# Kernel tuning notes

Measured on AMD Instinct MI355X. Metric: run time of the kernel, lower is better.

The kernel has to match this reference:

```python
import jax, jax.numpy as jnp
import numpy as np

B, N, K, D, L = 8, 1024, 16, 256, 3  # batch, max_node_num, neighbor fan-in, g_hidden_dim, layers


def setup_inputs() -> dict:
    key = jax.random.key(0)
    ks = jax.random.split(key, 14)
    f32 = jnp.float32
    scale = 1.0 / np.sqrt(D).astype(np.float32)
    randn = lambda k, s: jax.random.normal(k, s, dtype=f32)
    lens = jax.random.randint(ks[12], (B,), N // 2, N + 1)
    node_mask = (jnp.arange(N)[None, :] < lens[:, None]).astype(f32)
    return {
        "h0": randn(ks[0], (B, N, D)),
        "c0": randn(ks[1], (B, N, D)),
        "x_in": randn(ks[2], (B, N, D)),
        "x_out": randn(ks[3], (B, N, D)),
        "W_in": randn(ks[4], (4, D, D)) * scale,   # gates stacked: [i, o, f, cell]
        "U_in": randn(ks[5], (4, D, D)) * scale,
        "W_out": randn(ks[6], (4, D, D)) * scale,
        "U_out": randn(ks[7], (4, D, D)) * scale,
        "b": jnp.zeros((4, D), dtype=f32),
        "in_mask": jax.random.randint(ks[8], (B, N, K), 0, 2).astype(f32),
        "out_mask": jax.random.randint(ks[9], (B, N, K), 0, 2).astype(f32),
        "node_mask": node_mask,
        "in_nodes": jax.random.randint(ks[10], (B, N, K), 0, N, dtype=jnp.int32),
        "out_nodes": jax.random.randint(ks[11], (B, N, K), 0, N, dtype=jnp.int32),
        "num_layers": L,
    }


def _gather_agg(h, idx, nb_mask, node_mask):
    # h: [B,N,D], idx: [B,N,K] -> masked sum of neighbor hidden states [B,N,D]
    nb = jax.vmap(lambda hb, ib: hb[ib])(h, idx)           # [B,N,K,D]
    agg = jnp.einsum('bnkd,bnk->bnd', nb, nb_mask)
    return agg * node_mask[..., None]


def reference(h0, c0, x_in, x_out, W_in, U_in, W_out, U_out, b,
              in_mask, out_mask, node_mask, in_nodes, out_nodes, num_layers):
    h, c = h0, c0
    nm = node_mask[..., None]
    for _ in range(num_layers):
        h_in = _gather_agg(h, in_nodes, in_mask, node_mask)
        h_out = _gather_agg(h, out_nodes, out_mask, node_mask)
        # pre-activation for all 4 gates at once: [4,B,N,D]
        pre = (jnp.einsum('bnd,gde->gbne', x_in, W_in)
               + jnp.einsum('bnd,gde->gbne', h_in, U_in)
               + jnp.einsum('bnd,gde->gbne', x_out, W_out)
               + jnp.einsum('bnd,gde->gbne', h_out, U_out)
               + b[:, None, None, :])
        i_g = jax.nn.sigmoid(pre[0])
        o_g = jax.nn.sigmoid(pre[1])
        f_g = jax.nn.sigmoid(pre[2])
        g = jnp.tanh(pre[3])
        c = (f_g * c + i_g * g) * nm
        h = o_g * jnp.tanh(c) * nm
    return h
```

## Files before the change

### kernel.cpp

```cpp
#include <hip/hip_runtime.h>
#include <hip/hip_bf16.h>
#include <cstdint>
#include <cstddef>

typedef __hip_bfloat16 bf16;
typedef _Float16 f16;
typedef __attribute__((ext_vector_type(4))) float f32x4;
typedef __attribute__((ext_vector_type(8))) _Float16 f16x8;
typedef __attribute__((ext_vector_type(4))) _Float16 f16x4;
typedef __attribute__((ext_vector_type(4))) unsigned short u16x4;

#define BB 8
#define NN 1024
#define KK 16
#define DD 256
#define MM (BB * NN)
#define NLAYER 3

__device__ __forceinline__ float ldf(const void* p, size_t i, int isf32) {
  return isf32 ? ((const float*)p)[i] : __bfloat162float(((const bf16*)p)[i]);
}

__device__ __forceinline__ f32x4 ldf4(const void* p, size_t vi, int isf32) {
  f32x4 r;
  if (isf32) {
    r = ((const f32x4*)p)[vi];
  } else {
    u16x4 u = ((const u16x4*)p)[vi];
#pragma unroll
    for (int q = 0; q < 4; q++) {
      union { unsigned u; float f; } c;
      c.u = ((unsigned)u[q]) << 16;
      r[q] = c.f;
    }
  }
  return r;
}

__device__ __forceinline__ void gload_lds16(const void* g, void* l) {
  __builtin_amdgcn_global_load_lds(
      (const __attribute__((address_space(1))) unsigned int*)g,
      (__attribute__((address_space(3))) unsigned int*)l, 16, 0, 0);
}

__device__ __forceinline__ int detect_isf32_wave(const void* W) {
  int lane = threadIdx.x & 63;
  unsigned short b = ((const unsigned short*)W)[2 * lane];
  int e = (b >> 7) & 0xFF;
  int sane = ((e >= 105 && e <= 130) || (b & 0x7FFF) == 0) ? 1 : 0;
  unsigned long long m = __ballot(sane);
  return (__popcll(m) > 32) ? 0 : 1;
}

__device__ __forceinline__ float fsigmoid(float x) {
  float a = fminf(fmaxf(-1.44269504f * x, -126.f), 126.f);
  float e = __builtin_amdgcn_exp2f(a);
  return __builtin_amdgcn_rcpf(1.f + e);
}
__device__ __forceinline__ float ftanh(float x) {
  float a = fminf(fmaxf(2.88539008f * x, -126.f), 126.f);
  float e = __builtin_amdgcn_exp2f(a);
  return 1.f - 2.f * __builtin_amdgcn_rcpf(1.f + e);
}

struct Params {
  const void *h0, *c0, *x_in, *x_out, *W_in, *U_in, *W_out, *U_out, *bvec;
  const void *in_mask, *out_mask, *node_mask;
  const int *in_nodes, *out_nodes;
  float *biasI, *nmF, *inmF, *outmF;
  f16 *h_cur, *c_cur, *A_buf, *X_buf, *BT_W, *BT_U, *XW;
  void* outp;
};

#define PREP_VEC_TOTAL (256 + 2048 + 32768 + 32768 + 524288 + 524288)
#define PREP_BLOCKS (256 + (PREP_VEC_TOTAL + 255) / 256)
__global__ void prep_k(Params p) {
  __shared__ float tile[64][65];
  int isf32 = detect_isf32_wave(p.W_in);
  int b = blockIdx.x;
  int t = threadIdx.x;

  if (b < 256) {
    int bx = b & 3, by = (b >> 2) & 3, z = b >> 4;
    int g = z & 3, which = z >> 2;
    const void* src = (which == 0) ? p.W_in : (which == 1) ? p.W_out
                     : (which == 2) ? p.U_in : p.U_out;
    f16* dst = (which < 2) ? p.BT_W : p.BT_U;
    int colofs = (which & 1) * 256;
    size_t gbase = (size_t)g * DD * DD;
    int tx = t & 63, ty = t >> 6;
    int d0 = bx * 64, e0 = by * 64;
#pragma unroll
    for (int r = 0; r < 64; r += 4)
      tile[ty + r][tx] = ldf(src, gbase + (size_t)(d0 + ty + r) * DD + e0 + tx, isf32);
    __syncthreads();
#pragma unroll
    for (int r = 0; r < 64; r += 4)
      dst[(size_t)(4 * (e0 + ty + r) + g) * 512 + colofs + d0 + tx] = (f16)tile[tx][ty + r];
    return;
  }

  size_t i = (size_t)(b - 256) * 256 + t;
  const size_t V0 = 256;
  const size_t V1 = V0 + 2048;
  const size_t V2 = V1 + 32768;
  const size_t V3 = V2 + 32768;
  const size_t V4 = V3 + 524288;
  const size_t V5 = V4 + 524288;
  if (i < V0) {
    f32x4 r;
#pragma unroll
    for (int g = 0; g < 4; g++) r[g] = ldf(p.bvec, (size_t)g * 256 + i, isf32);
    ((f32x4*)p.biasI)[i] = r;
  } else if (i < V1) {
    ((f32x4*)p.nmF)[i - V0] = ldf4(p.node_mask, i - V0, isf32);
  } else if (i < V2) {
    ((f32x4*)p.inmF)[i - V1] = ldf4(p.in_mask, i - V1, isf32);
  } else if (i < V3) {
    ((f32x4*)p.outmF)[i - V2] = ldf4(p.out_mask, i - V2, isf32);
  } else if (i < V4) {
    size_t j = i - V3;
    f32x4 hv = ldf4(p.h0, j, isf32);
    f32x4 cv = ldf4(p.c0, j, isf32);
    f16x4 ho, co;
#pragma unroll
    for (int q = 0; q < 4; q++) { ho[q] = (f16)hv[q]; co[q] = (f16)cv[q]; }
    ((f16x4*)p.h_cur)[j] = ho;
    ((f16x4*)p.c_cur)[j] = co;
  } else if (i < V5) {
    size_t j = i - V4;
    size_t m = j >> 6, d4 = (j & 63) * 4;
    f32x4 xi = ldf4(p.x_in, j, isf32);
    f32x4 xo = ldf4(p.x_out, j, isf32);
    f16x4 a, bq;
#pragma unroll
    for (int q = 0; q < 4; q++) { a[q] = (f16)xi[q]; bq[q] = (f16)xo[q]; }
    *(f16x4*)(p.X_buf + m * 512 + d4)       = a;
    *(f16x4*)(p.X_buf + m * 512 + 256 + d4) = bq;
  }
}

__global__ void gather_k(Params p) {
  int wave = threadIdx.x >> 6;
  int lane = threadIdx.x & 63;
  int m = (blockIdx.x & 7) * 1024 + (blockIdx.x >> 3) * 4 + wave;
  int l5 = lane & 31, dir = lane >> 5;
  int myidx = 0; float mymask = 0.f;
  if (lane < 16)      { myidx = p.in_nodes[(size_t)m * KK + lane];
                        mymask = p.inmF[(size_t)m * KK + lane]; }
  else if (lane < 32) { myidx = p.out_nodes[(size_t)m * KK + lane - 16];
                        mymask = p.outmF[(size_t)m * KK + lane - 16]; }
  const f16* hb = p.h_cur + (size_t)(m >> 10) * NN * DD;
  float acc[8] = {};
#pragma unroll
  for (int k = 0; k < KK; k++) {
    int src = dir * 16 + k;
    int idxk = __shfl(myidx, src);
    float wk = __shfl(mymask, src);
    f16x8 v = *(const f16x8*)(hb + (size_t)idxk * DD + l5 * 8);
#pragma unroll
    for (int q = 0; q < 8; q++) acc[q] += wk * (float)v[q];
  }
  float nm = p.nmF[m];
  f16x8 o;
#pragma unroll
  for (int q = 0; q < 8; q++) o[q] = (f16)(acc[q] * nm);
  *(f16x8*)(p.A_buf + (size_t)m * 512 + dir * 256 + l5 * 8) = o;
}

__device__ __forceinline__ int mtile_of(int bx) { return (bx & 7) * 8 + (bx >> 3); }

template <int FIRST>
__global__ __launch_bounds__(256, 2)
void gemm_k(Params p, int last) {
  __shared__ __attribute__((aligned(16))) char smem[65536];
  float* tileF = (float*)smem;
  int isf32 = detect_isf32_wave(p.W_in);
  int t = threadIdx.x;
  int w = t >> 6, lane = t & 63;
  int wr = w >> 1, wc = w & 1;
  int row16 = lane & 15, kgrp = lane >> 4;
  int mBase = mtile_of(blockIdx.x) * 128, nBase = blockIdx.y * 128;

  int aoff[2][4], boff[2][4];
#pragma unroll
  for (int sub = 0; sub < 2; sub++) {
    int ch = ((sub * 4 + kgrp) ^ (row16 & 7)) * 8;
#pragma unroll
    for (int i = 0; i < 4; i++) aoff[sub][i] = (wr * 64 + 16 * i + row16) * 64 + ch;
#pragma unroll
    for (int j = 0; j < 4; j++) boff[sub][j] = (wc * 64 + 16 * j + row16) * 64 + ch;
  }
  int srow = t >> 3;
  int scol = ((t & 7) ^ (srow & 7)) * 8;
  const f16* gaH0 = p.A_buf + (size_t)(mBase + srow) * 512 + scol;
  const f16* gbU0 = p.BT_U + (size_t)(nBase + srow) * 512 + scol;
  const f16* gaX0 = p.X_buf + (size_t)(mBase + srow) * 512 + scol;
  const f16* gbW0 = p.BT_W + (size_t)(nBase + srow) * 512 + scol;

  const size_t xwkey = ((size_t)(blockIdx.y * 64 + blockIdx.x) * 256 + t) * 16;

  f32x4 acc[4][4];
  if (FIRST) {
#pragma unroll
    for (int i = 0; i < 4; i++)
#pragma unroll
      for (int j = 0; j < 4; j++) acc[i][j] = (f32x4){0.f, 0.f, 0.f, 0.f};
  } else {
    const f16x4* xw = (const f16x4*)p.XW + xwkey;
#pragma unroll
    for (int i = 0; i < 4; i++)
#pragma unroll
      for (int j = 0; j < 4; j++) {
        f16x4 v = xw[i * 4 + j];
#pragma unroll
        for (int r = 0; r < 4; r++) acc[i][j][r] = (float)v[r];
      }
  }

  const int NSTEP = FIRST ? 16 : 8;
  auto stage = [&](int it, int buf) {
    const f16* ga; const f16* gb; int kt;
    if (FIRST && it < 8) { ga = gaX0; gb = gbW0; kt = it * 64; }
    else                 { ga = gaH0; gb = gbU0; kt = (FIRST ? it - 8 : it) * 64; }
    f16* As = (f16*)(smem + buf * 32768);
    f16* Bs = (f16*)(smem + buf * 32768 + 16384);
#pragma unroll
    for (int q = 0; q < 4; q++)
      gload_lds16(ga + kt + (size_t)(32 * q) * 512, As + q * 2048 + t * 8);
#pragma unroll
    for (int q = 0; q < 4; q++)
      gload_lds16(gb + kt + (size_t)(32 * q) * 512, Bs + q * 2048 + t * 8);
  };

  stage(0, 0);
  __syncthreads();

#pragma unroll
  for (int it = 0; it < NSTEP; ++it) {
    int cur = it & 1;
    if (it < NSTEP - 1) stage(it + 1, cur ^ 1);
    f16* As = (f16*)(smem + cur * 32768);
    f16* Bs = (f16*)(smem + cur * 32768 + 16384);
#pragma unroll
    for (int sub = 0; sub < 2; sub++) {
      f16x8 af[4], bfr[4];
#pragma unroll
      for (int i = 0; i < 4; i++) af[i] = *(const f16x8*)(As + aoff[sub][i]);
#pragma unroll
      for (int j = 0; j < 4; j++) bfr[j] = *(const f16x8*)(Bs + boff[sub][j]);
#pragma unroll
      for (int i = 0; i < 4; i++)
#pragma unroll
        for (int j = 0; j < 4; j++)
          acc[i][j] = __builtin_amdgcn_mfma_f32_16x16x32_f16(af[i], bfr[j], acc[i][j], 0, 0, 0);
    }
    if (FIRST && it == 7) {
      float bb4[4];
#pragma unroll
      for (int j = 0; j < 4; j++) bb4[j] = p.biasI[nBase + wc * 64 + 16 * j + row16];
      f16x4* dst = (f16x4*)p.XW + xwkey;
#pragma unroll
      for (int i = 0; i < 4; i++)
#pragma unroll
        for (int j = 0; j < 4; j++) {
          f16x4 v;
#pragma unroll
          for (int r = 0; r < 4; r++) {
            acc[i][j][r] += bb4[j];
            v[r] = (f16)acc[i][j][r];
          }
          dst[i * 4 + j] = v;
        }
    }
    __syncthreads();
  }

#pragma unroll
  for (int pp = 0; pp < 2; pp++) {
    __syncthreads();
    if (wc == pp) {
#pragma unroll
      for (int i = 0; i < 4; i++)
#pragma unroll
        for (int j = 0; j < 4; j++) {
          int cl = 16 * j + row16;
#pragma unroll
          for (int r = 0; r < 4; r++) {
            int rr = wr * 64 + 16 * i + 4 * kgrp + r;
            int ch = (cl >> 2) ^ (rr & 7);
            tileF[rr * 64 + ch * 4 + (cl & 3)] = acc[i][j][r];
          }
        }
    }
    __syncthreads();
    int el = t & 15;
    int nb2 = nBase + 64 * pp;
    int eb = nb2 >> 2;
#pragma unroll
    for (int rep = 0; rep < 8; rep++) {
      int ml = rep * 16 + (t >> 4);
      int gm = mBase + ml;
      f32x4 vals = *(const f32x4*)(tileF + ml * 64 + ((el ^ (ml & 7))) * 4);
      float nm = p.nmF[gm];
      size_t ci = (size_t)gm * DD + eb + el;
      float cold = (float)p.c_cur[ci];
      float ig = fsigmoid(vals[0]);
      float og = fsigmoid(vals[1]);
      float fg = fsigmoid(vals[2]);
      float gg = ftanh(vals[3]);
      float cn = (fg * cold + ig * gg) * nm;
      float hn = og * ftanh(cn) * nm;
      p.c_cur[ci] = (f16)cn;
      p.h_cur[ci] = (f16)hn;
      if (last) {
        if (isf32) ((float*)p.outp)[ci] = hn;
        else       ((bf16*)p.outp)[ci] = __float2bfloat16(hn);
      }
    }
  }
}

extern "C" void kernel_launch(void* const* d_in, const int* in_sizes, int n_in,
                              void* d_out, int out_size, void* d_ws, size_t ws_size,
                              hipStream_t stream) {
  char* ws = (char*)d_ws;
  f16*   h_cur = (f16*)(ws + 256);
  f16*   c_cur = h_cur + (size_t)MM * DD;
  f16*   A_buf = c_cur + (size_t)MM * DD;
  f16*   X_buf = A_buf + (size_t)MM * 512;
  f16*   BT_W  = X_buf + (size_t)MM * 512;
  f16*   BT_U  = BT_W + (size_t)1024 * 512;
  f16*   XW    = BT_U + (size_t)1024 * 512;
  float* biasI = (float*)(XW + (size_t)MM * 1024);
  float* nmF   = biasI + 1024;
  float* inmF  = nmF + MM;
  float* outmF = inmF + (size_t)MM * KK;

  Params p;
  p.h0 = d_in[0]; p.c0 = d_in[1]; p.x_in = d_in[2]; p.x_out = d_in[3];
  p.W_in = d_in[4]; p.U_in = d_in[5]; p.W_out = d_in[6]; p.U_out = d_in[7];
  p.bvec = d_in[8]; p.in_mask = d_in[9]; p.out_mask = d_in[10]; p.node_mask = d_in[11];
  p.in_nodes = (const int*)d_in[12]; p.out_nodes = (const int*)d_in[13];
  p.biasI = biasI; p.nmF = nmF; p.inmF = inmF; p.outmF = outmF;
  p.h_cur = h_cur; p.c_cur = c_cur; p.A_buf = A_buf; p.X_buf = X_buf;
  p.BT_W = BT_W; p.BT_U = BT_U; p.XW = XW;
  p.outp = d_out;

  prep_k<<<PREP_BLOCKS, 256, 0, stream>>>(p);
  for (int l = 0; l < NLAYER; l++) {
    gather_k<<<MM / 4, 256, 0, stream>>>(p);
    if (l == 0) gemm_k<1><<<dim3(MM / 128, 8), 256, 0, stream>>>(p, l == NLAYER - 1);
    else        gemm_k<0><<<dim3(MM / 128, 8), 256, 0, stream>>>(p, l == NLAYER - 1);
  }
}
```

Before: 199.4 us.

## Fuse first-layer gather into prep and read masks and c0 directly from inputs

Folds the first layer's neighbor gather into the prep kernel, reading h0 directly in its original dtype, which removes one launch and the h0/c0 conversion pass. The float copies of the node, in and out masks are dropped; gather and the GEMM epilogue now read the masks through the dtype-aware loader. The first GEMM also reads c0 directly. This cuts prep-side memory traffic and one kernel launch, in exchange for wider uncoalesced fp32 gathers of h0 on the first layer.

```diff
diff --git a/kernel.cpp b/kernel.cpp
--- a/kernel.cpp
+++ b/kernel.cpp
@@ -9,6 +9,7 @@
 typedef __attribute__((ext_vector_type(8))) _Float16 f16x8;
 typedef __attribute__((ext_vector_type(4))) _Float16 f16x4;
 typedef __attribute__((ext_vector_type(4))) unsigned short u16x4;
+typedef __attribute__((ext_vector_type(8))) unsigned short u16x8;
 
 #define BB 8
 #define NN 1024
@@ -67,20 +68,77 @@
   const void *h0, *c0, *x_in, *x_out, *W_in, *U_in, *W_out, *U_out, *bvec;
   const void *in_mask, *out_mask, *node_mask;
   const int *in_nodes, *out_nodes;
-  float *biasI, *nmF, *inmF, *outmF;
+  float *biasI;
   f16 *h_cur, *c_cur, *A_buf, *X_buf, *BT_W, *BT_U, *XW;
   void* outp;
 };
 
-#define PREP_VEC_TOTAL (256 + 2048 + 32768 + 32768 + 524288 + 524288)
-#define PREP_BLOCKS (256 + (PREP_VEC_TOTAL + 255) / 256)
+template <int FIRST>
+__device__ __forceinline__ void gather_body(const Params& p, int b, int t, int isf32) {
+  int wave = t >> 6;
+  int lane = t & 63;
+  int m = (b & 7) * 1024 + (b >> 3) * 4 + wave;
+  int l5 = lane & 31, dir = lane >> 5;
+  int myidx = 0; float mymask = 0.f;
+  if (lane < 16)      { myidx = p.in_nodes[(size_t)m * KK + lane];
+                        mymask = ldf(p.in_mask, (size_t)m * KK + lane, isf32); }
+  else if (lane < 32) { myidx = p.out_nodes[(size_t)m * KK + lane - 16];
+                        mymask = ldf(p.out_mask, (size_t)m * KK + lane - 16, isf32); }
+  int bb = m >> 10;
+  float acc8[8] = {};
+#pragma unroll
+  for (int k = 0; k < KK; k++) {
+    int src = dir * 16 + k;
+    int idxk = __shfl(myidx, src);
+    float wk = __shfl(mymask, src);
+    if (FIRST) {
+      if (isf32) {
+        const float* hr = (const float*)p.h0 + ((size_t)bb * NN + idxk) * DD + l5 * 8;
+        f32x4 a = *(const f32x4*)hr, b2 = *(const f32x4*)(hr + 4);
+#pragma unroll
+        for (int q = 0; q < 4; q++) { acc8[q] += wk * a[q]; acc8[4 + q] += wk * b2[q]; }
+      } else {
+        const unsigned short* hr =
+            (const unsigned short*)p.h0 + ((size_t)bb * NN + idxk) * DD + l5 * 8;
+        u16x8 v = *(const u16x8*)hr;
+#pragma unroll
+        for (int q = 0; q < 8; q++) {
+          union { unsigned u; float f; } c; c.u = ((unsigned)v[q]) << 16;
+          acc8[q] += wk * c.f;
+        }
+      }
+    } else {
+      const f16* hr = p.h_cur + ((size_t)bb * NN + idxk) * DD + l5 * 8;
+      f16x8 v = *(const f16x8*)hr;
+#pragma unroll
+      for (int q = 0; q < 8; q++) acc8[q] += wk * (float)v[q];
+    }
+  }
+  float nm = ldf(p.node_mask, m, isf32);
+  f16x8 o;
+#pragma unroll
+  for (int q = 0; q < 8; q++) o[q] = (f16)(acc8[q] * nm);
+  *(f16x8*)(p.A_buf + (size_t)m * 512 + dir * 256 + l5 * 8) = o;
+}
+
+#define GATHER_BLOCKS 2048
+#define TRANS_BLOCKS 256
+#define VEC_TOTAL (256 + 524288)
+#define VEC_BLOCKS ((VEC_TOTAL + 255) / 256)
+#define PREP_BLOCKS (GATHER_BLOCKS + TRANS_BLOCKS + VEC_BLOCKS)
 __global__ void prep_k(Params p) {
   __shared__ float tile[64][65];
   int isf32 = detect_isf32_wave(p.W_in);
   int b = blockIdx.x;
   int t = threadIdx.x;
 
-  if (b < 256) {
+  if (b < GATHER_BLOCKS) {
+    gather_body<1>(p, b, t, isf32);
+    return;
+  }
+  b -= GATHER_BLOCKS;
+
+  if (b < TRANS_BLOCKS) {
     int bx = b & 3, by = (b >> 2) & 3, z = b >> 4;
     int g = z & 3, which = z >> 2;
     const void* src = (which == 0) ? p.W_in : (which == 1) ? p.W_out
@@ -99,36 +157,18 @@
       dst[(size_t)(4 * (e0 + ty + r) + g) * 512 + colofs + d0 + tx] = (f16)tile[tx][ty + r];
     return;
   }
-
-  size_t i = (size_t)(b - 256) * 256 + t;
+  b -= TRANS_BLOCKS;
+
+  size_t i = (size_t)b * 256 + t;
   const size_t V0 = 256;
-  const size_t V1 = V0 + 2048;
-  const size_t V2 = V1 + 32768;
-  const size_t V3 = V2 + 32768;
-  const size_t V4 = V3 + 524288;
-  const size_t V5 = V4 + 524288;
+  const size_t V1 = V0 + 524288;
   if (i < V0) {
     f32x4 r;
 #pragma unroll
     for (int g = 0; g < 4; g++) r[g] = ldf(p.bvec, (size_t)g * 256 + i, isf32);
     ((f32x4*)p.biasI)[i] = r;
   } else if (i < V1) {
-    ((f32x4*)p.nmF)[i - V0] = ldf4(p.node_mask, i - V0, isf32);
-  } else if (i < V2) {
-    ((f32x4*)p.inmF)[i - V1] = ldf4(p.in_mask, i - V1, isf32);
-  } else if (i < V3) {
-    ((f32x4*)p.outmF)[i - V2] = ldf4(p.out_mask, i - V2, isf32);
-  } else if (i < V4) {
-    size_t j = i - V3;
-    f32x4 hv = ldf4(p.h0, j, isf32);
-    f32x4 cv = ldf4(p.c0, j, isf32);
-    f16x4 ho, co;
-#pragma unroll
-    for (int q = 0; q < 4; q++) { ho[q] = (f16)hv[q]; co[q] = (f16)cv[q]; }
-    ((f16x4*)p.h_cur)[j] = ho;
-    ((f16x4*)p.c_cur)[j] = co;
-  } else if (i < V5) {
-    size_t j = i - V4;
+    size_t j = i - V0;
     size_t m = j >> 6, d4 = (j & 63) * 4;
     f32x4 xi = ldf4(p.x_in, j, isf32);
     f32x4 xo = ldf4(p.x_out, j, isf32);
@@ -141,31 +181,8 @@
 }
 
 __global__ void gather_k(Params p) {
-  int wave = threadIdx.x >> 6;
-  int lane = threadIdx.x & 63;
-  int m = (blockIdx.x & 7) * 1024 + (blockIdx.x >> 3) * 4 + wave;
-  int l5 = lane & 31, dir = lane >> 5;
-  int myidx = 0; float mymask = 0.f;
-  if (lane < 16)      { myidx = p.in_nodes[(size_t)m * KK + lane];
-                        mymask = p.inmF[(size_t)m * KK + lane]; }
-  else if (lane < 32) { myidx = p.out_nodes[(size_t)m * KK + lane - 16];
-                        mymask = p.outmF[(size_t)m * KK + lane - 16]; }
-  const f16* hb = p.h_cur + (size_t)(m >> 10) * NN * DD;
-  float acc[8] = {};
-#pragma unroll
-  for (int k = 0; k < KK; k++) {
-    int src = dir * 16 + k;
-    int idxk = __shfl(myidx, src);
-    float wk = __shfl(mymask, src);
-    f16x8 v = *(const f16x8*)(hb + (size_t)idxk * DD + l5 * 8);
-#pragma unroll
-    for (int q = 0; q < 8; q++) acc[q] += wk * (float)v[q];
-  }
-  float nm = p.nmF[m];
-  f16x8 o;
-#pragma unroll
-  for (int q = 0; q < 8; q++) o[q] = (f16)(acc[q] * nm);
-  *(f16x8*)(p.A_buf + (size_t)m * 512 + dir * 256 + l5 * 8) = o;
+  int isf32 = detect_isf32_wave(p.W_in);
+  gather_body<0>(p, blockIdx.x, threadIdx.x, isf32);
 }
 
 __device__ __forceinline__ int mtile_of(int bx) { return (bx & 7) * 8 + (bx >> 3); }
@@ -302,9 +319,9 @@
       int ml = rep * 16 + (t >> 4);
       int gm = mBase + ml;
       f32x4 vals = *(const f32x4*)(tileF + ml * 64 + ((el ^ (ml & 7))) * 4);
-      float nm = p.nmF[gm];
+      float nm = ldf(p.node_mask, gm, isf32);
       size_t ci = (size_t)gm * DD + eb + el;
-      float cold = (float)p.c_cur[ci];
+      float cold = FIRST ? ldf(p.c0, ci, isf32) : (float)p.c_cur[ci];
       float ig = fsigmoid(vals[0]);
       float og = fsigmoid(vals[1]);
       float fg = fsigmoid(vals[2]);
@@ -333,24 +350,21 @@
   f16*   BT_U  = BT_W + (size_t)1024 * 512;
   f16*   XW    = BT_U + (size_t)1024 * 512;
   float* biasI = (float*)(XW + (size_t)MM * 1024);
-  float* nmF   = biasI + 1024;
-  float* inmF  = nmF + MM;
-  float* outmF = inmF + (size_t)MM * KK;
 
   Params p;
   p.h0 = d_in[0]; p.c0 = d_in[1]; p.x_in = d_in[2]; p.x_out = d_in[3];
   p.W_in = d_in[4]; p.U_in = d_in[5]; p.W_out = d_in[6]; p.U_out = d_in[7];
   p.bvec = d_in[8]; p.in_mask = d_in[9]; p.out_mask = d_in[10]; p.node_mask = d_in[11];
   p.in_nodes = (const int*)d_in[12]; p.out_nodes = (const int*)d_in[13];
-  p.biasI = biasI; p.nmF = nmF; p.inmF = inmF; p.outmF = outmF;
+  p.biasI = biasI;
   p.h_cur = h_cur; p.c_cur = c_cur; p.A_buf = A_buf; p.X_buf = X_buf;
   p.BT_W = BT_W; p.BT_U = BT_U; p.XW = XW;
   p.outp = d_out;
 
   prep_k<<<PREP_BLOCKS, 256, 0, stream>>>(p);
-  for (int l = 0; l < NLAYER; l++) {
-    gather_k<<<MM / 4, 256, 0, stream>>>(p);
-    if (l == 0) gemm_k<1><<<dim3(MM / 128, 8), 256, 0, stream>>>(p, l == NLAYER - 1);
-    else        gemm_k<0><<<dim3(MM / 128, 8), 256, 0, stream>>>(p, l == NLAYER - 1);
-  }
-}
+  gemm_k<1><<<dim3(MM / 128, 8), 256, 0, stream>>>(p, 0);
+  gather_k<<<GATHER_BLOCKS, 256, 0, stream>>>(p);
+  gemm_k<0><<<dim3(MM / 128, 8), 256, 0, stream>>>(p, 0);
+  gather_k<<<GATHER_BLOCKS, 256, 0, stream>>>(p);
+  gemm_k<0><<<dim3(MM / 128, 8), 256, 0, stream>>>(p, 1);
+}
```

Result: slower. 203.8 us (+2.2%).
